# Kernel optimization log

Hardware: AMD Instinct MI355X
Metric: run time of the kernel (lower is better)

Reference implementation:

```python
import jax, jax.numpy as jnp
import numpy as np

B, S, D, H = 2, 2048, 2048, 16
HD = D // H  # head_dim = 128
ALIBI_BIAS_MAX = 8


def alibi_bias(n_heads, seq_len, alibi_bias_max=8, dtype=jnp.float32):
    # matches torch alibi_bias(full=False): shape [1, H, 1, S]
    dist = jnp.arange(1 - seq_len, 1, dtype=dtype).reshape(1, 1, 1, seq_len)
    m = jnp.arange(1, n_heads + 1, dtype=dtype) * (alibi_bias_max / n_heads)
    slopes = (1.0 / 2.0 ** m).reshape(1, n_heads, 1, 1)
    return dist * slopes


def setup_inputs() -> dict:
    key = jax.random.key(0)
    k1, k2, k3, k4, k5 = jax.random.split(key, 5)
    x = jax.random.normal(k1, (B, S, D), dtype=jnp.float32)
    # ALiBi additive bias, as produced by TritonFlashCausalAttention.attn_mask_
    attn_mask = alibi_bias(H, S, ALIBI_BIAS_MAX, jnp.float32)  # [1,H,1,S]
    scale = 1.0 / np.sqrt(D)
    Wqkv = jax.random.normal(k2, (D, 3 * D), dtype=jnp.float32) * scale
    bqkv = jnp.zeros((3 * D,), dtype=jnp.float32)
    Wout = jax.random.normal(k3, (D, D), dtype=jnp.float32) * scale
    bout = jnp.zeros((D,), dtype=jnp.float32)
    return {"x": x, "attn_mask": attn_mask, "Wqkv": Wqkv, "bqkv": bqkv,
            "Wout": Wout, "bout": bout}


def reference(x, attn_mask, Wqkv, bqkv, Wout, bout):
    b, s, d = x.shape
    # fused QKV projection
    qkv = x @ Wqkv + bqkv                       # [B,S,3D]
    qkv = qkv.reshape(b, s, 3, H, HD)
    q, k, v = qkv[:, :, 0], qkv[:, :, 1], qkv[:, :, 2]  # each [B,S,H,HD]
    softmax_scale = 1.0 / jnp.sqrt(jnp.asarray(HD, dtype=x.dtype))
    scores = jnp.einsum('bshd,bthd->bhst', q, k) * softmax_scale  # [B,H,S,S]
    scores = scores + attn_mask                  # ALiBi bias [1,H,1,S]
    causal = jnp.tril(jnp.ones((s, s), dtype=bool))
    scores = jnp.where(causal, scores, jnp.asarray(-jnp.inf, dtype=scores.dtype))
    attn = jax.nn.softmax(scores, axis=-1)
    out = jnp.einsum('bhst,bthd->bshd', attn, v).reshape(b, s, d)
    return out @ Wout + bout
```

## Files before the change

### kernel.cpp

```cpp
#include <hip/hip_runtime.h>
#include <hip/hip_bf16.h>

typedef __bf16 bf16x8 __attribute__((ext_vector_type(8)));
typedef float f32x4 __attribute__((ext_vector_type(4)));
typedef unsigned short u16;

constexpr int BATCH = 2, SEQ = 2048, DM = 2048, NH = 16, HD = 128;
constexpr int N3 = 3 * DM;
constexpr int MROWS = BATCH * SEQ;

__device__ __forceinline__ u16 f2bf(float f) {
  unsigned u = __builtin_bit_cast(unsigned, f);
  unsigned r = 0x7FFFu + ((u >> 16) & 1u);
  return (u16)((u + r) >> 16);
}

__device__ __forceinline__ void glds16(const u16* g, u16* l) {
  __builtin_amdgcn_global_load_lds(
      (const __attribute__((address_space(1))) unsigned*)(const void*)g,
      (__attribute__((address_space(3))) unsigned*)(void*)l, 16, 0, 0);
}

__global__ __launch_bounds__(256) void k_cvt(const float* __restrict__ in,
                                             u16* __restrict__ out, int n4) {
  int i = blockIdx.x * blockDim.x + threadIdx.x;
  if (i >= n4) return;
  float4 v = reinterpret_cast<const float4*>(in)[i];
  ushort4 o;
  o.x = f2bf(v.x); o.y = f2bf(v.y); o.z = f2bf(v.z); o.w = f2bf(v.w);
  reinterpret_cast<ushort4*>(out)[i] = o;
}

__global__ __launch_bounds__(256) void k_transpose(const float* __restrict__ in,
                                                   u16* __restrict__ out, int K, int N) {
  __shared__ float tile[32][33];
  int n0 = blockIdx.x * 32, k0 = blockIdx.y * 32;
  int tx = threadIdx.x & 31, ty = threadIdx.x >> 5;
#pragma unroll
  for (int r = ty; r < 32; r += 8) tile[r][tx] = in[(long)(k0 + r) * N + n0 + tx];
  __syncthreads();
#pragma unroll
  for (int r = ty; r < 32; r += 8) out[(long)(n0 + r) * K + k0 + tx] = f2bf(tile[tx][r]);
}

__global__ __launch_bounds__(512) void k_gemm_qkv(const u16* __restrict__ A,
                                                  const u16* __restrict__ Bt,
                                                  const float* __restrict__ bias,
                                                  u16* __restrict__ Qb, u16* __restrict__ Kb,
                                                  u16* __restrict__ Vt) {
  constexpr int K = DM;
  constexpr int NKT = K / 64;
  constexpr int NIT = NKT / 2;
  __shared__ u16 LA[2 * 256 * 64];
  __shared__ u16 LB[2 * 256 * 64];
  int m0 = blockIdx.y * 256, n0 = blockIdx.x * 256;
  int t = threadIdx.x, lane = t & 63, w = t >> 6;
  int l15 = lane & 15, lhi = lane >> 4;
  int wrow = w >> 2, wcol = w & 3;
  int srow = t >> 3;
  int scol = ((t & 7) ^ (srow & 7)) * 8;

#define STG_A(TILE, HALF) do {                                                   \
    int kb_ = ((TILE) < NKT ? (TILE) : NKT - 1) * 64;                            \
    u16* d_ = LA + (((TILE) & 1) * 16384 + (HALF) * 8192 + w * 512);             \
    glds16(A + (long)(m0 + (HALF) * 128 + srow) * K + kb_ + scol, d_);           \
    glds16(A + (long)(m0 + (HALF) * 128 + 64 + srow) * K + kb_ + scol, d_ + 4096); \
  } while (0)
#define STG_B(TILE, HALF) do {                                                   \
    int kb_ = ((TILE) < NKT ? (TILE) : NKT - 1) * 64;                            \
    u16* d_ = LB + (((TILE) & 1) * 16384 + (HALF) * 8192 + w * 512);             \
    glds16(Bt + (long)(n0 + (HALF) * 128 + srow) * K + kb_ + scol, d_);          \
    glds16(Bt + (long)(n0 + (HALF) * 128 + 64 + srow) * K + kb_ + scol, d_ + 4096); \
  } while (0)

  bf16x8 af[4][2], bfr[4][2];
  f32x4 acc[8][4] = {};

#define LDA_FRAGS(BUF, QM) do {                                                  \
    _Pragma("unroll") for (int mi = 0; mi < 4; mi++) {                           \
      int rA = wrow * 128 + ((QM) * 4 + mi) * 16 + l15;                          \
      _Pragma("unroll") for (int kk = 0; kk < 2; kk++)                           \
        af[mi][kk] = *(const bf16x8*)(LA + (BUF) * 16384 + rA * 64 +             \
                                      (((kk * 4 + lhi) ^ (rA & 7)) * 8));        \
    } } while (0)
#define LDB_FRAGS(BUF, QN) do {                                                  \
    _Pragma("unroll") for (int ni = 0; ni < 2; ni++) {                           \
      int rB = wcol * 64 + ((QN) * 2 + ni) * 16 + l15;                           \
      _Pragma("unroll") for (int kk = 0; kk < 2; kk++)                           \
        bfr[(QN) * 2 + ni][kk] = *(const bf16x8*)(LB + (BUF) * 16384 + rB * 64 + \
                                      (((kk * 4 + lhi) ^ (rB & 7)) * 8));        \
    } } while (0)
#define MM(QM, QN) do {                                                          \
    __builtin_amdgcn_s_setprio(1);                                               \
    _Pragma("unroll") for (int mi = 0; mi < 4; mi++)                             \
    _Pragma("unroll") for (int ni = 0; ni < 2; ni++)                             \
    _Pragma("unroll") for (int kk = 0; kk < 2; kk++)                             \
      acc[(QM) * 4 + mi][(QN) * 2 + ni] = __builtin_amdgcn_mfma_f32_16x16x32_bf16( \
          af[mi][kk], bfr[(QN) * 2 + ni][kk], acc[(QM) * 4 + mi][(QN) * 2 + ni], 0, 0, 0); \
    __builtin_amdgcn_s_setprio(0);                                               \
  } while (0)
#define BAR __builtin_amdgcn_s_barrier()
#define VMW4 do { asm volatile("s_waitcnt vmcnt(4)" ::: "memory");               \
                  __builtin_amdgcn_sched_barrier(0); } while (0)

  STG_A(0, 0); STG_A(0, 1); STG_B(0, 0); STG_B(0, 1);
  STG_B(1, 0); STG_B(1, 1);
  VMW4; BAR;

  for (int it = 0; it < NIT; it++) {
    int k1 = 2 * it + 1, k2 = 2 * it + 2, k3 = 2 * it + 3;
    LDA_FRAGS(0, 0); LDB_FRAGS(0, 0); STG_A(k1, 0);       BAR; MM(0, 0); BAR;
    LDB_FRAGS(0, 1);                  STG_A(k1, 1);       BAR; MM(0, 1); BAR;
    LDA_FRAGS(0, 1);                  STG_B(k2, 0);       BAR; MM(1, 0); BAR;
                                      STG_B(k2, 1); VMW4; BAR; MM(1, 1); BAR;
    LDA_FRAGS(1, 0); LDB_FRAGS(1, 0); STG_A(k2, 0);       BAR; MM(0, 0); BAR;
    LDB_FRAGS(1, 1);                  STG_A(k2, 1);       BAR; MM(0, 1); BAR;
    LDA_FRAGS(1, 1);                  STG_B(k3, 0);       BAR; MM(1, 0); BAR;
                                      STG_B(k3, 1); VMW4; BAR; MM(1, 1); BAR;
  }
#undef STG_A
#undef STG_B
#undef LDA_FRAGS
#undef LDB_FRAGS
#undef MM
#undef BAR
#undef VMW4

#pragma unroll
  for (int mi = 0; mi < 8; mi++)
#pragma unroll
    for (int ni = 0; ni < 4; ni++) {
      int col = n0 + wcol * 64 + ni * 16 + l15;
      float bv = bias[col];
      int sec = col >> 11, dn = col & 2047, h = dn >> 7, hd = dn & 127;
#pragma unroll
      for (int r = 0; r < 4; r++) {
        int row = m0 + wrow * 128 + mi * 16 + lhi * 4 + r;
        int bb = row >> 11, ss = row & 2047;
        u16 val = f2bf(acc[mi][ni][r] + bv);
        if (sec == 0)
          Qb[(((long)(bb * NH + h)) * SEQ + ss) * HD + hd] = val;
        else if (sec == 1)
          Kb[(((long)(bb * NH + h)) * SEQ + ss) * HD + hd] = val;
        else
          Vt[(((long)(bb * NH + h)) * HD + hd) * SEQ + ss] = val;
      }
    }
}

__global__ __launch_bounds__(256) void k_gemm_out(const u16* __restrict__ A,
                                                  const u16* __restrict__ Bt,
                                                  const float* __restrict__ bias,
                                                  float* __restrict__ Out) {
  constexpr int K = DM, N = DM;
  __shared__ u16 As[128 * 32], Bs[128 * 32];
  int m0 = blockIdx.y * 128, n0 = blockIdx.x * 128;
  int t = threadIdx.x, lane = t & 63, w = t >> 6;
  int l15 = lane & 15, lhi = lane >> 4;
  int wr = (w >> 1) * 64, wc = (w & 1) * 64;
  int srow = t >> 2, sk = (t & 3) * 8;
  const u16* Ap0 = A + (long)(m0 + srow) * K + sk;
  const u16* Ap1 = A + (long)(m0 + 64 + srow) * K + sk;
  const u16* Bp0 = Bt + (long)(n0 + srow) * K + sk;
  const u16* Bp1 = Bt + (long)(n0 + 64 + srow) * K + sk;
  u16* AsW0 = As + w * 512; u16* AsW1 = As + 2048 + w * 512;
  u16* BsW0 = Bs + w * 512; u16* BsW1 = Bs + 2048 + w * 512;

  f32x4 acc[4][4] = {};
  for (int k0 = 0; k0 < K; k0 += 32) {
    glds16(Ap0 + k0, AsW0);
    glds16(Ap1 + k0, AsW1);
    glds16(Bp0 + k0, BsW0);
    glds16(Bp1 + k0, BsW1);
    __syncthreads();
    bf16x8 af[4], bg[4];
#pragma unroll
    for (int i = 0; i < 4; i++) af[i] = *(const bf16x8*)(As + (wr + i * 16 + l15) * 32 + lhi * 8);
#pragma unroll
    for (int j = 0; j < 4; j++) bg[j] = *(const bf16x8*)(Bs + (wc + j * 16 + l15) * 32 + lhi * 8);
#pragma unroll
    for (int i = 0; i < 4; i++)
#pragma unroll
      for (int j = 0; j < 4; j++)
        acc[i][j] = __builtin_amdgcn_mfma_f32_16x16x32_bf16(af[i], bg[j], acc[i][j], 0, 0, 0);
    __syncthreads();
  }
#pragma unroll
  for (int i = 0; i < 4; i++)
#pragma unroll
    for (int j = 0; j < 4; j++) {
      int col = n0 + wc + j * 16 + l15;
      float bv = bias[col];
#pragma unroll
      for (int r = 0; r < 4; r++) {
        int row = m0 + wr + i * 16 + lhi * 4 + r;
        Out[(long)row * N + col] = acc[i][j][r] + bv;
      }
    }
}

__global__ __launch_bounds__(256) void k_attn(const u16* __restrict__ Qb,
                                              const u16* __restrict__ Kb,
                                              const u16* __restrict__ Vt,
                                              const float* __restrict__ mask,
                                              u16* __restrict__ Ao) {
  constexpr int NT = SEQ / 64;
  int bh = blockIdx.y;
  int qp = blockIdx.x;
  int t = threadIdx.x, w = t >> 6, lane = t & 63;
  int l15 = lane & 15, lhi = lane >> 4;
  int b = bh >> 4, h = bh & 15;
  const u16* Qh = Qb + (long)bh * SEQ * HD;
  const u16* Kh = Kb + (long)bh * SEQ * HD;
  const u16* Vh = Vt + (long)bh * HD * SEQ;
  const float* mh = mask + h * SEQ;

  __shared__ u16 Ks[64 * 128];
  __shared__ u16 Vs[128 * 64];
  __shared__ u16 p_lds[4 * 16 * 64];
  u16* pw = p_lds + w * (16 * 64);

  int krow[4], kcol[4], vrow[4], vcol[4];
#pragma unroll
  for (int i = 0; i < 4; i++) {
    int c = i * 256 + t;
    krow[i] = c >> 4; kcol[i] = (c & 15) * 8;
    vrow[i] = c >> 3; vcol[i] = (c & 7) * 8;
  }

  const float sm_scale = 0.08838834764831845f;

  for (int half = 0; half < 2; half++) {
    int qt = half ? qp : (NT - 1 - qp);
    int q0 = qt * 64 + w * 16;
    int nt = qt + 1;

    bf16x8 qf[4];
#pragma unroll
    for (int kc = 0; kc < 4; kc++)
      qf[kc] = *(const bf16x8*)(Qh + (long)(q0 + l15) * HD + kc * 32 + lhi * 8);

    int rowr[4];
#pragma unroll
    for (int r = 0; r < 4; r++) rowr[r] = q0 + lhi * 4 + r;

    float mrun[4], lrun[4];
    f32x4 oacc[8] = {};
#pragma unroll
    for (int r = 0; r < 4; r++) { mrun[r] = -1e30f; lrun[r] = 0.f; }

    bf16x8 kst[4], vst[4];
#pragma unroll
    for (int i = 0; i < 4; i++) kst[i] = *(const bf16x8*)(Kh + (long)krow[i] * HD + kcol[i]);
#pragma unroll
    for (int i = 0; i < 4; i++) vst[i] = *(const bf16x8*)(Vh + (long)vrow[i] * SEQ + vcol[i]);
    __syncthreads();
#pragma unroll
    for (int i = 0; i < 4; i++)
      *(bf16x8*)(Ks + krow[i] * 128 + (kcol[i] ^ ((krow[i] & 7) << 3))) = kst[i];
#pragma unroll
    for (int i = 0; i < 4; i++)
      *(bf16x8*)(Vs + vrow[i] * 64 + (vcol[i] ^ ((vrow[i] & 7) << 3))) = vst[i];
    __syncthreads();

    for (int kt = 0; kt < nt; kt++) {
      int kb = kt * 64;
      bool have_next = (kt + 1 < nt);
      bool diag = (kt == nt - 1);
      if (have_next) {
        int kb2 = kb + 64;
#pragma unroll
        for (int i = 0; i < 4; i++)
          kst[i] = *(const bf16x8*)(Kh + (long)(kb2 + krow[i]) * HD + kcol[i]);
#pragma unroll
        for (int i = 0; i < 4; i++)
          vst[i] = *(const bf16x8*)(Vh + (long)vrow[i] * SEQ + kb2 + vcol[i]);
      }
      float bvv[4];
#pragma unroll
      for (int cb = 0; cb < 4; cb++) bvv[cb] = mh[kb + cb * 16 + l15];
      f32x4 sc[4] = {};
      __builtin_amdgcn_s_setprio(1);
#pragma unroll
      for (int kc = 0; kc < 4; kc++)
#pragma unroll
        for (int cb = 0; cb < 4; cb++) {
          int rr = cb * 16 + l15;
          bf16x8 kf = *(const bf16x8*)(Ks + rr * 128 + ((kc * 32 + lhi * 8) ^ ((rr & 7) << 3)));
          sc[cb] = __builtin_amdgcn_mfma_f32_16x16x32_bf16(qf[kc], kf, sc[cb], 0, 0, 0);
        }
      __builtin_amdgcn_s_setprio(0);
      float p[4][4], tmax[4];
#pragma unroll
      for (int cb = 0; cb < 4; cb++) {
        int col = kb + cb * 16 + l15;
#pragma unroll
        for (int r = 0; r < 4; r++) {
          float v = sc[cb][r] * sm_scale + bvv[cb];
          if (diag) v = (col <= rowr[r]) ? v : -1e30f;
          p[cb][r] = v;
        }
      }
#pragma unroll
      for (int r = 0; r < 4; r++)
        tmax[r] = fmaxf(fmaxf(p[0][r], p[1][r]), fmaxf(p[2][r], p[3][r]));
      float alpha[4];
#pragma unroll
      for (int r = 0; r < 4; r++) {
        float v = tmax[r];
        v = fmaxf(v, __shfl_xor(v, 1));
        v = fmaxf(v, __shfl_xor(v, 2));
        v = fmaxf(v, __shfl_xor(v, 4));
        v = fmaxf(v, __shfl_xor(v, 8));
        float mnew = fmaxf(mrun[r], v);
        alpha[r] = __expf(mrun[r] - mnew);
        mrun[r] = mnew;
        float s = 0.f;
#pragma unroll
        for (int cb = 0; cb < 4; cb++) {
          float e = __expf(p[cb][r] - mnew);
          p[cb][r] = e;
          s += e;
        }
        s += __shfl_xor(s, 1); s += __shfl_xor(s, 2);
        s += __shfl_xor(s, 4); s += __shfl_xor(s, 8);
        lrun[r] = lrun[r] * alpha[r] + s;
      }
#pragma unroll
      for (int nb = 0; nb < 8; nb++)
#pragma unroll
        for (int r = 0; r < 4; r++) oacc[nb][r] *= alpha[r];
#pragma unroll
      for (int cb = 0; cb < 4; cb++)
#pragma unroll
        for (int r = 0; r < 4; r++) {
          int rr = lhi * 4 + r;
          pw[(rr * 64 + cb * 16 + l15) ^ ((rr & 7) << 3)] = f2bf(p[cb][r]);
        }
      asm volatile("s_waitcnt lgkmcnt(0)" ::: "memory");
      bf16x8 pa0 = *(const bf16x8*)(pw + ((l15 * 64 + lhi * 8) ^ ((l15 & 7) << 3)));
      bf16x8 pa1 = *(const bf16x8*)(pw + ((l15 * 64 + 32 + lhi * 8) ^ ((l15 & 7) << 3)));
      __builtin_amdgcn_s_setprio(1);
#pragma unroll
      for (int nb = 0; nb < 8; nb++) {
        int rr = nb * 16 + l15;
        bf16x8 vf0 = *(const bf16x8*)(Vs + rr * 64 + ((lhi * 8) ^ ((rr & 7) << 3)));
        bf16x8 vf1 = *(const bf16x8*)(Vs + rr * 64 + ((32 + lhi * 8) ^ ((rr & 7) << 3)));
        oacc[nb] = __builtin_amdgcn_mfma_f32_16x16x32_bf16(pa0, vf0, oacc[nb], 0, 0, 0);
        oacc[nb] = __builtin_amdgcn_mfma_f32_16x16x32_bf16(pa1, vf1, oacc[nb], 0, 0, 0);
      }
      __builtin_amdgcn_s_setprio(0);
      if (have_next) {
        __syncthreads();
#pragma unroll
        for (int i = 0; i < 4; i++)
          *(bf16x8*)(Ks + krow[i] * 128 + (kcol[i] ^ ((krow[i] & 7) << 3))) = kst[i];
#pragma unroll
        for (int i = 0; i < 4; i++)
          *(bf16x8*)(Vs + vrow[i] * 64 + (vcol[i] ^ ((vrow[i] & 7) << 3))) = vst[i];
        __syncthreads();
      }
    }
#pragma unroll
    for (int nb = 0; nb < 8; nb++)
#pragma unroll
      for (int r = 0; r < 4; r++) {
        int row = q0 + lhi * 4 + r;
        float v = oacc[nb][r] / lrun[r];
        Ao[((long)(b * SEQ + row)) * DM + h * HD + nb * 16 + l15] = f2bf(v);
      }
  }
}

extern "C" void kernel_launch(void* const* d_in, const int* in_sizes, int n_in,
                              void* d_out, int out_size, void* d_ws, size_t ws_size,
                              hipStream_t stream) {
  const float* x    = (const float*)d_in[0];
  const float* amsk = (const float*)d_in[1];
  const float* Wqkv = (const float*)d_in[2];
  const float* bqkv = (const float*)d_in[3];
  const float* Wout = (const float*)d_in[4];
  const float* bout = (const float*)d_in[5];
  float* out = (float*)d_out;

  char* ws = (char*)d_ws;
  u16* xb  = (u16*)(ws + 0);
  u16* WqT = (u16*)(ws + 16777216UL);
  u16* WoT = (u16*)(ws + 41943040UL);
  u16* Qb  = (u16*)(ws + 50331648UL);
  u16* Kb  = (u16*)(ws + 67108864UL);
  u16* Vt  = (u16*)(ws + 83886080UL);
  u16* Ao  = (u16*)(ws + 100663296UL);

  k_cvt<<<8192, 256, 0, stream>>>(x, xb, (MROWS * DM) / 4);
  k_transpose<<<dim3(N3 / 32, DM / 32), 256, 0, stream>>>(Wqkv, WqT, DM, N3);
  k_transpose<<<dim3(DM / 32, DM / 32), 256, 0, stream>>>(Wout, WoT, DM, DM);
  k_gemm_qkv<<<dim3(N3 / 256, MROWS / 256), 512, 0, stream>>>(xb, WqT, bqkv, Qb, Kb, Vt);
  k_attn<<<dim3(SEQ / 128, BATCH * NH), 256, 0, stream>>>(Qb, Kb, Vt, amsk, Ao);
  k_gemm_out<<<dim3(DM / 128, MROWS / 128), 256, 0, stream>>>(Ao, WoT, bout, out);
}
```

Baseline: 325.6 us.

## Shrink QKV GEMM N-tile to 192 for even wave count across CUs

Changes the QKV projection GEMM block tile from 256x256 to 256x192, so the grid becomes 512 blocks instead of 384, aiming for balanced waves over the CUs and removing the tail from a partial wave. The B staging, fragment loads and MFMA phases are restructured for three 16-column fragments per wave, and explicit LDS-count waits are added before the MFMA phases. The smaller tile lowers arithmetic intensity per block, adds extra barrier/wait overhead, and makes the phase schedule less symmetric.

```diff
diff --git a/kernel.cpp b/kernel.cpp
--- a/kernel.cpp
+++ b/kernel.cpp
@@ -52,85 +52,104 @@
   constexpr int NKT = K / 64;
   constexpr int NIT = NKT / 2;
   __shared__ u16 LA[2 * 256 * 64];
-  __shared__ u16 LB[2 * 256 * 64];
-  int m0 = blockIdx.y * 256, n0 = blockIdx.x * 256;
+  __shared__ u16 LB[2 * 192 * 64];
+  int m0 = blockIdx.y * 256, n0 = blockIdx.x * 192;
   int t = threadIdx.x, lane = t & 63, w = t >> 6;
   int l15 = lane & 15, lhi = lane >> 4;
   int wrow = w >> 2, wcol = w & 3;
   int srow = t >> 3;
   int scol = ((t & 7) ^ (srow & 7)) * 8;
 
-#define STG_A(TILE, HALF) do {                                                   \
-    int kb_ = ((TILE) < NKT ? (TILE) : NKT - 1) * 64;                            \
-    u16* d_ = LA + (((TILE) & 1) * 16384 + (HALF) * 8192 + w * 512);             \
-    glds16(A + (long)(m0 + (HALF) * 128 + srow) * K + kb_ + scol, d_);           \
+#define STG_A(TILE, HALF) do {                                                     \
+    int kb_ = ((TILE) < NKT ? (TILE) : NKT - 1) * 64;                              \
+    u16* d_ = LA + (((TILE) & 1) * 16384 + (HALF) * 8192 + w * 512);               \
+    glds16(A + (long)(m0 + (HALF) * 128 + srow) * K + kb_ + scol, d_);             \
     glds16(A + (long)(m0 + (HALF) * 128 + 64 + srow) * K + kb_ + scol, d_ + 4096); \
   } while (0)
-#define STG_B(TILE, HALF) do {                                                   \
-    int kb_ = ((TILE) < NKT ? (TILE) : NKT - 1) * 64;                            \
-    u16* d_ = LB + (((TILE) & 1) * 16384 + (HALF) * 8192 + w * 512);             \
-    glds16(Bt + (long)(n0 + (HALF) * 128 + srow) * K + kb_ + scol, d_);          \
-    glds16(Bt + (long)(n0 + (HALF) * 128 + 64 + srow) * K + kb_ + scol, d_ + 4096); \
+#define STG_B(TILE) do {                                                           \
+    int kb_ = ((TILE) < NKT ? (TILE) : NKT - 1) * 64;                              \
+    u16* d_ = LB + (((TILE) & 1) * 12288 + w * 512);                               \
+    glds16(Bt + (long)(n0 + srow) * K + kb_ + scol, d_);                           \
+    glds16(Bt + (long)(n0 + 64 + srow) * K + kb_ + scol, d_ + 4096);               \
+    glds16(Bt + (long)(n0 + 128 + srow) * K + kb_ + scol, d_ + 8192);              \
   } while (0)
 
-  bf16x8 af[4][2], bfr[4][2];
-  f32x4 acc[8][4] = {};
-
-#define LDA_FRAGS(BUF, QM) do {                                                  \
-    _Pragma("unroll") for (int mi = 0; mi < 4; mi++) {                           \
-      int rA = wrow * 128 + ((QM) * 4 + mi) * 16 + l15;                          \
-      _Pragma("unroll") for (int kk = 0; kk < 2; kk++)                           \
-        af[mi][kk] = *(const bf16x8*)(LA + (BUF) * 16384 + rA * 64 +             \
-                                      (((kk * 4 + lhi) ^ (rA & 7)) * 8));        \
+  bf16x8 af[4][2], bfr[3][2];
+  f32x4 acc[8][3] = {};
+
+#define LDA_FRAGS(BUF, QM) do {                                                    \
+    _Pragma("unroll") for (int mi = 0; mi < 4; mi++) {                             \
+      int rA = wrow * 128 + ((QM) * 4 + mi) * 16 + l15;                            \
+      _Pragma("unroll") for (int kk = 0; kk < 2; kk++)                             \
+        af[mi][kk] = *(const bf16x8*)(LA + (BUF) * 16384 + rA * 64 +               \
+                                      (((kk * 4 + lhi) ^ (rA & 7)) * 8));          \
     } } while (0)
-#define LDB_FRAGS(BUF, QN) do {                                                  \
-    _Pragma("unroll") for (int ni = 0; ni < 2; ni++) {                           \
-      int rB = wcol * 64 + ((QN) * 2 + ni) * 16 + l15;                           \
-      _Pragma("unroll") for (int kk = 0; kk < 2; kk++)                           \
-        bfr[(QN) * 2 + ni][kk] = *(const bf16x8*)(LB + (BUF) * 16384 + rB * 64 + \
-                                      (((kk * 4 + lhi) ^ (rB & 7)) * 8));        \
+#define LDB_FRAGS01(BUF) do {                                                      \
+    _Pragma("unroll") for (int ni = 0; ni < 2; ni++) {                             \
+      int rB = wcol * 48 + ni * 16 + l15;                                          \
+      _Pragma("unroll") for (int kk = 0; kk < 2; kk++)                             \
+        bfr[ni][kk] = *(const bf16x8*)(LB + (BUF) * 12288 + rB * 64 +              \
+                                       (((kk * 4 + lhi) ^ (rB & 7)) * 8));         \
     } } while (0)
-#define MM(QM, QN) do {                                                          \
-    __builtin_amdgcn_s_setprio(1);                                               \
-    _Pragma("unroll") for (int mi = 0; mi < 4; mi++)                             \
-    _Pragma("unroll") for (int ni = 0; ni < 2; ni++)                             \
-    _Pragma("unroll") for (int kk = 0; kk < 2; kk++)                             \
-      acc[(QM) * 4 + mi][(QN) * 2 + ni] = __builtin_amdgcn_mfma_f32_16x16x32_bf16( \
-          af[mi][kk], bfr[(QN) * 2 + ni][kk], acc[(QM) * 4 + mi][(QN) * 2 + ni], 0, 0, 0); \
-    __builtin_amdgcn_s_setprio(0);                                               \
+#define LDB_FRAGS2(BUF) do {                                                       \
+    int rB = wcol * 48 + 2 * 16 + l15;                                             \
+    _Pragma("unroll") for (int kk = 0; kk < 2; kk++)                               \
+      bfr[2][kk] = *(const bf16x8*)(LB + (BUF) * 12288 + rB * 64 +                 \
+                                    (((kk * 4 + lhi) ^ (rB & 7)) * 8));            \
+  } while (0)
+#define MM2(QM) do {                                                               \
+    __builtin_amdgcn_s_setprio(1);                                                 \
+    _Pragma("unroll") for (int mi = 0; mi < 4; mi++)                               \
+    _Pragma("unroll") for (int ni = 0; ni < 2; ni++)                               \
+    _Pragma("unroll") for (int kk = 0; kk < 2; kk++)                               \
+      acc[(QM) * 4 + mi][ni] = __builtin_amdgcn_mfma_f32_16x16x32_bf16(            \
+          af[mi][kk], bfr[ni][kk], acc[(QM) * 4 + mi][ni], 0, 0, 0);               \
+    __builtin_amdgcn_s_setprio(0);                                                 \
+  } while (0)
+#define MM1(QM) do {                                                               \
+    __builtin_amdgcn_s_setprio(1);                                                 \
+    _Pragma("unroll") for (int mi = 0; mi < 4; mi++)                               \
+    _Pragma("unroll") for (int kk = 0; kk < 2; kk++)                               \
+      acc[(QM) * 4 + mi][2] = __builtin_amdgcn_mfma_f32_16x16x32_bf16(             \
+          af[mi][kk], bfr[2][kk], acc[(QM) * 4 + mi][2], 0, 0, 0);                 \
+    __builtin_amdgcn_s_setprio(0);                                                 \
   } while (0)
 #define BAR __builtin_amdgcn_s_barrier()
-#define VMW4 do { asm volatile("s_waitcnt vmcnt(4)" ::: "memory");               \
+#define LG0 do { asm volatile("s_waitcnt lgkmcnt(0)" ::: "memory");                \
+                 __builtin_amdgcn_sched_barrier(0); } while (0)
+#define VMW3 do { asm volatile("s_waitcnt vmcnt(3)" ::: "memory");                 \
                   __builtin_amdgcn_sched_barrier(0); } while (0)
 
-  STG_A(0, 0); STG_A(0, 1); STG_B(0, 0); STG_B(0, 1);
-  STG_B(1, 0); STG_B(1, 1);
-  VMW4; BAR;
+  STG_A(0, 0); STG_A(0, 1); STG_B(0); STG_B(1);
+  VMW3; BAR;
 
   for (int it = 0; it < NIT; it++) {
     int k1 = 2 * it + 1, k2 = 2 * it + 2, k3 = 2 * it + 3;
-    LDA_FRAGS(0, 0); LDB_FRAGS(0, 0); STG_A(k1, 0);       BAR; MM(0, 0); BAR;
-    LDB_FRAGS(0, 1);                  STG_A(k1, 1);       BAR; MM(0, 1); BAR;
-    LDA_FRAGS(0, 1);                  STG_B(k2, 0);       BAR; MM(1, 0); BAR;
-                                      STG_B(k2, 1); VMW4; BAR; MM(1, 1); BAR;
-    LDA_FRAGS(1, 0); LDB_FRAGS(1, 0); STG_A(k2, 0);       BAR; MM(0, 0); BAR;
-    LDB_FRAGS(1, 1);                  STG_A(k2, 1);       BAR; MM(0, 1); BAR;
-    LDA_FRAGS(1, 1);                  STG_B(k3, 0);       BAR; MM(1, 0); BAR;
-                                      STG_B(k3, 1); VMW4; BAR; MM(1, 1); BAR;
+    LDA_FRAGS(0, 0); LDB_FRAGS01(0); STG_A(k1, 0);   BAR; LG0; MM2(0); BAR;
+    LDB_FRAGS2(0);                   STG_A(k1, 1);   BAR; LG0; MM1(0); BAR;
+    LDA_FRAGS(0, 1);                 STG_B(k2);      BAR; LG0; MM2(1); BAR;
+    VMW3;                                            BAR;      MM1(1); BAR;
+    LDA_FRAGS(1, 0); LDB_FRAGS01(1); STG_A(k2, 0);   BAR; LG0; MM2(0); BAR;
+    LDB_FRAGS2(1);                   STG_A(k2, 1);   BAR; LG0; MM1(0); BAR;
+    LDA_FRAGS(1, 1);                 STG_B(k3);      BAR; LG0; MM2(1); BAR;
+    VMW3;                                            BAR;      MM1(1); BAR;
   }
 #undef STG_A
 #undef STG_B
 #undef LDA_FRAGS
-#undef LDB_FRAGS
-#undef MM
+#undef LDB_FRAGS01
+#undef LDB_FRAGS2
+#undef MM2
+#undef MM1
 #undef BAR
-#undef VMW4
+#undef LG0
+#undef VMW3
 
 #pragma unroll
   for (int mi = 0; mi < 8; mi++)
 #pragma unroll
-    for (int ni = 0; ni < 4; ni++) {
-      int col = n0 + wcol * 64 + ni * 16 + l15;
+    for (int ni = 0; ni < 3; ni++) {
+      int col = n0 + wcol * 48 + ni * 16 + l15;
       float bv = bias[col];
       int sec = col >> 11, dn = col & 2047, h = dn >> 7, hd = dn & 127;
 #pragma unroll
@@ -395,7 +414,7 @@
   k_cvt<<<8192, 256, 0, stream>>>(x, xb, (MROWS * DM) / 4);
   k_transpose<<<dim3(N3 / 32, DM / 32), 256, 0, stream>>>(Wqkv, WqT, DM, N3);
   k_transpose<<<dim3(DM / 32, DM / 32), 256, 0, stream>>>(Wout, WoT, DM, DM);
-  k_gemm_qkv<<<dim3(N3 / 256, MROWS / 256), 512, 0, stream>>>(xb, WqT, bqkv, Qb, Kb, Vt);
+  k_gemm_qkv<<<dim3(N3 / 192, MROWS / 256), 512, 0, stream>>>(xb, WqT, bqkv, Qb, Kb, Vt);
   k_attn<<<dim3(SEQ / 128, BATCH * NH), 256, 0, stream>>>(Qb, Kb, Vt, amsk, Ao);
   k_gemm_out<<<dim3(DM / 128, MROWS / 128), 256, 0, stream>>>(Ao, WoT, bout, out);
 }
```

Result: faster. 307.1 us (-5.7%).
